# Performance work log

Measured on AMD Instinct MI355X. Metric: run time of the kernel, lower is better.

## Reference

```python
import jax, jax.numpy as jnp
import numpy as np

EPS = 1e-12
ETA = 1.0


def _l2norm(x, eps=EPS):
    # torch F.normalize: x / max(||x||, eps)
    n = jnp.sqrt(jnp.sum(x * x, axis=-1, keepdims=True))
    return x / jnp.maximum(n, eps)


def setup_inputs() -> dict:
    key = jax.random.key(0)
    ks = jax.random.split(key, 7)
    B, IN, H = 256, 512, 512
    std = 1.0 / np.sqrt(H)
    return {
        "inputs": jax.random.normal(ks[0], (B, IN), jnp.float32),
        "hidden": jax.random.normal(ks[1], (B, H), jnp.float32),
        "assoc_mem": jax.random.normal(ks[2], (B, H, H), jnp.float32),
        "W_ih": jax.random.uniform(ks[3], (3 * H, IN), jnp.float32, -std, std),
        "b_ih": jax.random.uniform(ks[4], (3 * H,), jnp.float32, -std, std),
        "W_hh": jax.random.uniform(ks[5], (3 * H, H), jnp.float32, -std, std),
        "b_hh": jax.random.uniform(ks[6], (3 * H,), jnp.float32, -std, std),
    }


def reference(inputs, hidden, assoc_mem, W_ih, b_ih, W_hh, b_hh):
    H = hidden.shape[-1]
    # projections = ih(inputs) + hh(hidden)  -> [B, 3H]
    proj = inputs @ W_ih.T + b_ih + hidden @ W_hh.T + b_hh
    u_gate, r, x_emb = jnp.split(proj, 3, axis=1)

    # rotation_operator(x_emb, r): Householder-style rotation in span{u, v}
    u = _l2norm(x_emb)                                    # [B, H]
    r_n = _l2norm(r)
    costh = jnp.sum(u * r_n, axis=-1, keepdims=True)      # [B, 1]
    sinth = jnp.sqrt(1.0 - costh ** 2)                    # [B, 1]
    v = _l2norm(r - jnp.sum(u * r, axis=-1, keepdims=True) * u)

    # R = I - uu^T - vv^T + tmp^T Rth tmp
    #   = I + (cos-1)(uu^T + vv^T) + sin (v u^T - u v^T)
    uu = jnp.einsum('bi,bj->bij', u, u)
    vv = jnp.einsum('bi,bj->bij', v, v)
    cross = jnp.einsum('bi,bj->bij', v, u) - jnp.einsum('bi,bj->bij', u, v)
    R = (jnp.eye(H, dtype=hidden.dtype)
         + (costh - 1.0)[..., None] * (uu + vv)
         + sinth[..., None] * cross)                      # [B, H, H]

    # Rth = assoc_mem @ R ; hidden_new = Rth @ hidden
    Rth_full = jnp.einsum('bij,bjk->bik', assoc_mem, R)
    hidden_new = jnp.einsum('bij,bj->bi', Rth_full, hidden)

    c = jax.nn.relu(hidden_new + x_emb)
    new_h = u_gate * hidden + (1.0 - u_gate) * c
    new_h = _l2norm(new_h) * ETA
    return new_h
```

## Files before the change

kernel.cpp:

```cpp
#include <hip/hip_runtime.h>


#define EPSF 1e-12f

typedef float vfloat4 __attribute__((ext_vector_type(4)));

__global__ __launch_bounds__(256) void gemm_proj(
    const float* __restrict__ inp, const float* __restrict__ hid,
    const float* __restrict__ W_ih, const float* __restrict__ W_hh,
    const float* __restrict__ b_ih, const float* __restrict__ b_hh,
    float* __restrict__ proj)
{
    __shared__ float Xs[32 * 34];
    __shared__ float Ws[32 * 64];
    const int t  = threadIdx.x;
    const int tx = t & 15;
    const int ty = t >> 4;
    const int col0 = blockIdx.x * 64;
    const int row0 = blockIdx.y * 32;
    const int lr = t >> 3;
    const int lk = (t & 7) * 4;

    float acc[2][4] = {};

    float4 xv  = *(const float4*)(inp  + (size_t)(row0 + lr) * 512 + lk);
    float4 wv0 = *(const float4*)(W_ih + (size_t)(col0 + lr) * 512 + lk);
    float4 wv1 = *(const float4*)(W_ih + (size_t)(col0 + lr + 32) * 512 + lk);

    for (int cc = 0; cc < 32; ++cc) {
        __syncthreads();
        Xs[(lk + 0) * 34 + lr] = xv.x;
        Xs[(lk + 1) * 34 + lr] = xv.y;
        Xs[(lk + 2) * 34 + lr] = xv.z;
        Xs[(lk + 3) * 34 + lr] = xv.w;
        Ws[(lk + 0) * 64 + lr] = wv0.x;
        Ws[(lk + 1) * 64 + lr] = wv0.y;
        Ws[(lk + 2) * 64 + lr] = wv0.z;
        Ws[(lk + 3) * 64 + lr] = wv0.w;
        Ws[(lk + 0) * 64 + lr + 32] = wv1.x;
        Ws[(lk + 1) * 64 + lr + 32] = wv1.y;
        Ws[(lk + 2) * 64 + lr + 32] = wv1.z;
        Ws[(lk + 3) * 64 + lr + 32] = wv1.w;

        const int nc = (cc < 31) ? cc + 1 : 31;
        const float* Xg = (nc & 16) ? hid  : inp;
        const float* Wg = (nc & 16) ? W_hh : W_ih;
        const int k0 = (nc & 15) * 32;
        xv  = *(const float4*)(Xg + (size_t)(row0 + lr) * 512 + k0 + lk);
        wv0 = *(const float4*)(Wg + (size_t)(col0 + lr) * 512 + k0 + lk);
        wv1 = *(const float4*)(Wg + (size_t)(col0 + lr + 32) * 512 + k0 + lk);

        __syncthreads();
#pragma unroll
        for (int kk = 0; kk < 32; ++kk) {
            float2 xv2 = *(const float2*)&Xs[kk * 34 + 2 * ty];
            float4 wv4 = *(const float4*)&Ws[kk * 64 + 4 * tx];
            acc[0][0] += xv2.x * wv4.x;
            acc[0][1] += xv2.x * wv4.y;
            acc[0][2] += xv2.x * wv4.z;
            acc[0][3] += xv2.x * wv4.w;
            acc[1][0] += xv2.y * wv4.x;
            acc[1][1] += xv2.y * wv4.y;
            acc[1][2] += xv2.y * wv4.z;
            acc[1][3] += xv2.y * wv4.w;
        }
    }

    const float4 bi = *(const float4*)(b_ih + col0 + 4 * tx);
    const float4 bh = *(const float4*)(b_hh + col0 + 4 * tx);
    const float4 bias = { bi.x + bh.x, bi.y + bh.y, bi.z + bh.z, bi.w + bh.w };
#pragma unroll
    for (int i = 0; i < 2; ++i) {
        const int r = row0 + 2 * ty + i;
        float4 o = { acc[i][0] + bias.x, acc[i][1] + bias.y,
                     acc[i][2] + bias.z, acc[i][3] + bias.w };
        *(float4*)(proj + (size_t)r * 1536 + col0 + 4 * tx) = o;
    }
}


__device__ __forceinline__ float4 block_reduce4_1024(float4 v, float4* red, int t) {
    __syncthreads();
#pragma unroll
    for (int off = 32; off >= 1; off >>= 1) {
        v.x += __shfl_xor(v.x, off, 64);
        v.y += __shfl_xor(v.y, off, 64);
        v.z += __shfl_xor(v.z, off, 64);
        v.w += __shfl_xor(v.w, off, 64);
    }
    if ((t & 63) == 0) red[t >> 6] = v;
    __syncthreads();
    float4 s = {0.f, 0.f, 0.f, 0.f};
#pragma unroll
    for (int i = 0; i < 16; ++i) {
        float4 r = red[i];
        s.x += r.x; s.y += r.y; s.z += r.z; s.w += r.w;
    }
    return s;
}

__global__ __launch_bounds__(1024) void rum_fused(
    const float* __restrict__ proj, const float* __restrict__ hid,
    const float* __restrict__ A, float* __restrict__ out)
{
    __shared__ float4 Rh4[128];
    __shared__ float  hn[512];
    __shared__ float4 red[16];
    float* Rh = (float*)Rh4;

    const int b = blockIdx.x;
    const int t = threadIdx.x;
    const float* prow = proj + (size_t)b * 1536;

    float xe = 0.f, rr = 0.f, hh = 0.f;
    if (t < 512) {
        xe = prow[1024 + t];
        rr = prow[512 + t];
        hh = hid[(size_t)b * 512 + t];
    }
    float4 p1 = { xe * xe, rr * rr, xe * rr, xe * hh };
    p1 = block_reduce4_1024(p1, red, t);
    const float nx = fmaxf(sqrtf(p1.x), EPSF);
    const float nr = fmaxf(sqrtf(p1.y), EPSF);
    const float costh = p1.z / (nx * nr);
    const float sinth = sqrtf(fmaxf(1.0f - costh * costh, 0.0f));
    const float dot_ur = p1.z / nx;
    const float a = p1.w / nx;
    const float u = xe / nx;
    const float w = rr - dot_ur * u;

    float4 p2 = { w * w, w * hh, 0.f, 0.f };
    p2 = block_reduce4_1024(p2, red, t);
    const float nw = fmaxf(sqrtf(p2.x), EPSF);
    const float bb = p2.y / nw;
    const float v = w / nw;
    const float cm1 = costh - 1.0f;
    if (t < 512)
        Rh[t] = hh + cm1 * (a * u + bb * v) + sinth * (a * v - bb * u);
    __syncthreads();

    const int lane = t & 63;
    const int wv = t >> 6;
    const int g = lane >> 4;
    const int c = lane & 15;

    float4 xr[8];
#pragma unroll
    for (int k = 0; k < 8; ++k) xr[k] = Rh4[c + 16 * k];

    const vfloat4* Ab = (const vfloat4*)(A + (size_t)b * 512 * 512);
#pragma unroll 2
    for (int q = 0; q < 8; ++q) {
        const int i = 32 * wv + 4 * q + g;
        const vfloat4* Ar = Ab + (size_t)i * 128;
        float a0 = 0.f, a1 = 0.f, a2 = 0.f, a3 = 0.f;
#pragma unroll
        for (int k = 0; k < 8; k += 4) {
            vfloat4 v0 = __builtin_nontemporal_load(Ar + c + 16 * (k + 0));
            vfloat4 v1 = __builtin_nontemporal_load(Ar + c + 16 * (k + 1));
            vfloat4 v2 = __builtin_nontemporal_load(Ar + c + 16 * (k + 2));
            vfloat4 v3 = __builtin_nontemporal_load(Ar + c + 16 * (k + 3));
            a0 += v0.x * xr[k + 0].x + v0.y * xr[k + 0].y + v0.z * xr[k + 0].z + v0.w * xr[k + 0].w;
            a1 += v1.x * xr[k + 1].x + v1.y * xr[k + 1].y + v1.z * xr[k + 1].z + v1.w * xr[k + 1].w;
            a2 += v2.x * xr[k + 2].x + v2.y * xr[k + 2].y + v2.z * xr[k + 2].z + v2.w * xr[k + 2].w;
            a3 += v3.x * xr[k + 3].x + v3.y * xr[k + 3].y + v3.z * xr[k + 3].z + v3.w * xr[k + 3].w;
        }
        float accq = (a0 + a1) + (a2 + a3);
#pragma unroll
        for (int off = 8; off >= 1; off >>= 1)
            accq += __shfl_xor(accq, off, 16);
        if (c == 0) hn[i] = accq;
    }
    __syncthreads();

    float tv = 0.f, ug = 0.f;
    if (t < 512) {
        ug = prow[t];
        const float cx = fmaxf(hn[t] + xe, 0.0f);
        tv = ug * hh + (1.0f - ug) * cx;
    }
    float4 p3 = { tv * tv, 0.f, 0.f, 0.f };
    p3 = block_reduce4_1024(p3, red, t);
    const float inv = 1.0f / fmaxf(sqrtf(p3.x), EPSF);
    if (t < 512)
        out[(size_t)b * 512 + t] = tv * inv;
}

extern "C" void kernel_launch(void* const* d_in, const int* in_sizes, int n_in,
                              void* d_out, int out_size, void* d_ws, size_t ws_size,
                              hipStream_t stream)
{
    const float* inp  = (const float*)d_in[0];
    const float* hid  = (const float*)d_in[1];
    const float* A    = (const float*)d_in[2];
    const float* W_ih = (const float*)d_in[3];
    const float* b_ih = (const float*)d_in[4];
    const float* W_hh = (const float*)d_in[5];
    const float* b_hh = (const float*)d_in[6];
    float* out = (float*)d_out;

    float* proj = (float*)d_ws;

    gemm_proj<<<dim3(24, 8), 256, 0, stream>>>(inp, hid, W_ih, W_hh, b_ih, b_hh, proj);
    rum_fused<<<dim3(256), 1024, 0, stream>>>(proj, hid, A, out);
}
```

Before: 385.8 us.

## Split per-batch matvec across two 512-thread blocks with register prefetch

Splits the fused per-batch kernel into a matvec kernel launched over (2, batch) blocks of 512 threads, each handling half the rows of the associative memory, and a separate epilogue kernel for the gate and final normalization. Row loads are software double-buffered in registers so the next row group's loads are in flight during the current dot products. This is meant to raise parallelism and memory-level concurrency on the 256 MB bandwidth-bound stream. The cost is that the rotation-vector reductions are recomputed by both halves, plus an extra launch and a global round trip for the intermediate hidden vector.

```diff
diff --git a/kernel.cpp b/kernel.cpp
--- a/kernel.cpp
+++ b/kernel.cpp
@@ -4,6 +4,26 @@
 #define EPSF 1e-12f
 
 typedef float vfloat4 __attribute__((ext_vector_type(4)));
+
+__device__ __forceinline__ float4 block_reduce4_512(float4 v, float4* red, int t) {
+    __syncthreads();
+#pragma unroll
+    for (int off = 32; off >= 1; off >>= 1) {
+        v.x += __shfl_xor(v.x, off, 64);
+        v.y += __shfl_xor(v.y, off, 64);
+        v.z += __shfl_xor(v.z, off, 64);
+        v.w += __shfl_xor(v.w, off, 64);
+    }
+    if ((t & 63) == 0) red[t >> 6] = v;
+    __syncthreads();
+    float4 s = {0.f, 0.f, 0.f, 0.f};
+#pragma unroll
+    for (int i = 0; i < 8; ++i) {
+        float4 r = red[i];
+        s.x += r.x; s.y += r.y; s.z += r.z; s.w += r.w;
+    }
+    return s;
+}
 
 __global__ __launch_bounds__(256) void gemm_proj(
     const float* __restrict__ inp, const float* __restrict__ hid,
@@ -78,48 +98,25 @@
     }
 }
 
-
-__device__ __forceinline__ float4 block_reduce4_1024(float4 v, float4* red, int t) {
-    __syncthreads();
-#pragma unroll
-    for (int off = 32; off >= 1; off >>= 1) {
-        v.x += __shfl_xor(v.x, off, 64);
-        v.y += __shfl_xor(v.y, off, 64);
-        v.z += __shfl_xor(v.z, off, 64);
-        v.w += __shfl_xor(v.w, off, 64);
-    }
-    if ((t & 63) == 0) red[t >> 6] = v;
-    __syncthreads();
-    float4 s = {0.f, 0.f, 0.f, 0.f};
-#pragma unroll
-    for (int i = 0; i < 16; ++i) {
-        float4 r = red[i];
-        s.x += r.x; s.y += r.y; s.z += r.z; s.w += r.w;
-    }
-    return s;
-}
-
-__global__ __launch_bounds__(1024) void rum_fused(
+__global__ __launch_bounds__(512) void matvec_half(
     const float* __restrict__ proj, const float* __restrict__ hid,
-    const float* __restrict__ A, float* __restrict__ out)
+    const float* __restrict__ A, float* __restrict__ hn)
 {
     __shared__ float4 Rh4[128];
-    __shared__ float  hn[512];
-    __shared__ float4 red[16];
+    __shared__ float4 red[8];
     float* Rh = (float*)Rh4;
 
-    const int b = blockIdx.x;
+    const int half = blockIdx.x;
+    const int b = blockIdx.y;
     const int t = threadIdx.x;
     const float* prow = proj + (size_t)b * 1536;
 
-    float xe = 0.f, rr = 0.f, hh = 0.f;
-    if (t < 512) {
-        xe = prow[1024 + t];
-        rr = prow[512 + t];
-        hh = hid[(size_t)b * 512 + t];
-    }
+    const float xe = prow[1024 + t];
+    const float rr = prow[512 + t];
+    const float hh = hid[(size_t)b * 512 + t];
+
     float4 p1 = { xe * xe, rr * rr, xe * rr, xe * hh };
-    p1 = block_reduce4_1024(p1, red, t);
+    p1 = block_reduce4_512(p1, red, t);
     const float nx = fmaxf(sqrtf(p1.x), EPSF);
     const float nr = fmaxf(sqrtf(p1.y), EPSF);
     const float costh = p1.z / (nx * nr);
@@ -130,13 +127,12 @@
     const float w = rr - dot_ur * u;
 
     float4 p2 = { w * w, w * hh, 0.f, 0.f };
-    p2 = block_reduce4_1024(p2, red, t);
+    p2 = block_reduce4_512(p2, red, t);
     const float nw = fmaxf(sqrtf(p2.x), EPSF);
     const float bb = p2.y / nw;
     const float v = w / nw;
     const float cm1 = costh - 1.0f;
-    if (t < 512)
-        Rh[t] = hh + cm1 * (a * u + bb * v) + sinth * (a * v - bb * u);
+    Rh[t] = hh + cm1 * (a * u + bb * v) + sinth * (a * v - bb * u);
     __syncthreads();
 
     const int lane = t & 63;
@@ -149,41 +145,62 @@
     for (int k = 0; k < 8; ++k) xr[k] = Rh4[c + 16 * k];
 
     const vfloat4* Ab = (const vfloat4*)(A + (size_t)b * 512 * 512);
-#pragma unroll 2
+    const int row_base = 256 * half + 32 * wv + g;
+
+    vfloat4 cur[8], nxt[8];
+    {
+        const vfloat4* Ar = Ab + (size_t)(row_base) * 128 + c;
+#pragma unroll
+        for (int k = 0; k < 8; ++k)
+            cur[k] = __builtin_nontemporal_load(Ar + 16 * k);
+    }
+#pragma unroll
     for (int q = 0; q < 8; ++q) {
-        const int i = 32 * wv + 4 * q + g;
-        const vfloat4* Ar = Ab + (size_t)i * 128;
-        float a0 = 0.f, a1 = 0.f, a2 = 0.f, a3 = 0.f;
-#pragma unroll
-        for (int k = 0; k < 8; k += 4) {
-            vfloat4 v0 = __builtin_nontemporal_load(Ar + c + 16 * (k + 0));
-            vfloat4 v1 = __builtin_nontemporal_load(Ar + c + 16 * (k + 1));
-            vfloat4 v2 = __builtin_nontemporal_load(Ar + c + 16 * (k + 2));
-            vfloat4 v3 = __builtin_nontemporal_load(Ar + c + 16 * (k + 3));
-            a0 += v0.x * xr[k + 0].x + v0.y * xr[k + 0].y + v0.z * xr[k + 0].z + v0.w * xr[k + 0].w;
-            a1 += v1.x * xr[k + 1].x + v1.y * xr[k + 1].y + v1.z * xr[k + 1].z + v1.w * xr[k + 1].w;
-            a2 += v2.x * xr[k + 2].x + v2.y * xr[k + 2].y + v2.z * xr[k + 2].z + v2.w * xr[k + 2].w;
-            a3 += v3.x * xr[k + 3].x + v3.y * xr[k + 3].y + v3.z * xr[k + 3].z + v3.w * xr[k + 3].w;
+        if (q < 7) {
+            const vfloat4* Ar = Ab + (size_t)(row_base + 4 * (q + 1)) * 128 + c;
+#pragma unroll
+            for (int k = 0; k < 8; ++k)
+                nxt[k] = __builtin_nontemporal_load(Ar + 16 * k);
         }
-        float accq = (a0 + a1) + (a2 + a3);
+        float a0 = 0.f, a1 = 0.f;
+#pragma unroll
+        for (int k = 0; k < 8; k += 2) {
+            a0 += cur[k].x * xr[k].x + cur[k].y * xr[k].y
+                + cur[k].z * xr[k].z + cur[k].w * xr[k].w;
+            a1 += cur[k + 1].x * xr[k + 1].x + cur[k + 1].y * xr[k + 1].y
+                + cur[k + 1].z * xr[k + 1].z + cur[k + 1].w * xr[k + 1].w;
+        }
+        float accq = a0 + a1;
 #pragma unroll
         for (int off = 8; off >= 1; off >>= 1)
             accq += __shfl_xor(accq, off, 16);
-        if (c == 0) hn[i] = accq;
-    }
-    __syncthreads();
-
-    float tv = 0.f, ug = 0.f;
-    if (t < 512) {
-        ug = prow[t];
-        const float cx = fmaxf(hn[t] + xe, 0.0f);
-        tv = ug * hh + (1.0f - ug) * cx;
-    }
-    float4 p3 = { tv * tv, 0.f, 0.f, 0.f };
-    p3 = block_reduce4_1024(p3, red, t);
-    const float inv = 1.0f / fmaxf(sqrtf(p3.x), EPSF);
-    if (t < 512)
-        out[(size_t)b * 512 + t] = tv * inv;
+        if (c == 0) hn[(size_t)b * 512 + row_base + 4 * q] = accq;
+#pragma unroll
+        for (int k = 0; k < 8; ++k) cur[k] = nxt[k];
+    }
+}
+
+__global__ __launch_bounds__(512) void epilogue512(
+    const float* __restrict__ proj, const float* __restrict__ hid,
+    const float* __restrict__ hn, float* __restrict__ out)
+{
+    __shared__ float4 red[8];
+    const int b = blockIdx.x;
+    const int t = threadIdx.x;
+    const float* prow = proj + (size_t)b * 1536;
+
+    const float ug = prow[t];
+    const float xe = prow[1024 + t];
+    const float hh = hid[(size_t)b * 512 + t];
+    const float hv = hn[(size_t)b * 512 + t];
+
+    const float cx = fmaxf(hv + xe, 0.0f);
+    const float tv = ug * hh + (1.0f - ug) * cx;
+
+    float4 p = { tv * tv, 0.f, 0.f, 0.f };
+    p = block_reduce4_512(p, red, t);
+    const float inv = 1.0f / fmaxf(sqrtf(p.x), EPSF);
+    out[(size_t)b * 512 + t] = tv * inv;
 }
 
 extern "C" void kernel_launch(void* const* d_in, const int* in_sizes, int n_in,
@@ -200,7 +217,9 @@
     float* out = (float*)d_out;
 
     float* proj = (float*)d_ws;
+    float* hn   = proj + 256 * 1536;
 
     gemm_proj<<<dim3(24, 8), 256, 0, stream>>>(inp, hid, W_ih, W_hh, b_ih, b_hh, proj);
-    rum_fused<<<dim3(256), 1024, 0, stream>>>(proj, hid, A, out);
-}
+    matvec_half<<<dim3(2, 256), 512, 0, stream>>>(proj, hid, A, hn);
+    epilogue512<<<dim3(256), 512, 0, stream>>>(proj, hid, hn, out);
+}
```

Result: no change. 386.5 us (+0.2%).
